# Kernel optimization log

Hardware: AMD Instinct MI355X
Metric: run time of the kernel (lower is better)

## Reference

```python
import jax, jax.numpy as jnp
import numpy as np

IN_F, OUT_F, N_PAIRS, BATCH = 1024, 1024, 4096, 32768
EPS = 1e-5

def setup_inputs() -> dict:
    key = jax.random.key(0)
    ks = jax.random.split(key, 8)
    x = jax.random.normal(ks[0], (BATCH, IN_F), dtype=jnp.float32)
    idx_i = jax.random.randint(ks[1], (N_PAIRS,), 0, IN_F)
    idx_j = jax.random.randint(ks[2], (N_PAIRS,), 0, IN_F)
    bound_lc = 1.0 / np.sqrt(N_PAIRS)
    bound_w1 = 1.0 / np.sqrt(IN_F)
    lw = jax.random.uniform(ks[3], (OUT_F, N_PAIRS), minval=-bound_lc, maxval=bound_lc, dtype=jnp.float32)
    w1 = jax.random.uniform(ks[4], (OUT_F, IN_F), minval=-bound_w1, maxval=bound_w1, dtype=jnp.float32)
    scale = jnp.ones((1, IN_F), dtype=jnp.float32)
    translation = jnp.zeros((1, IN_F), dtype=jnp.float32)
    gamma = jnp.ones((OUT_F,), dtype=jnp.float32)
    beta = jnp.zeros((OUT_F,), dtype=jnp.float32)
    return {"x": x, "idx_i": idx_i, "idx_j": idx_j, "scale": scale,
            "translation": translation, "lw": lw, "w1": w1,
            "gamma": gamma, "beta": beta}

def reference(x, idx_i, idx_j, scale, translation, lw, w1, gamma, beta):
    # levicivita transform: affine-normalize, gather pairs, multiply, GEMM
    xs = (x - translation) / scale                       # [B, in]
    pp = xs[:, idx_i] * xs[:, idx_j]                     # [B, num_pairs]
    lc = pp @ lw.T                                       # [B, out]
    base = x @ w1.T                                      # [B, out]
    c = lc + base
    # LayerNorm over last dim (eps=1e-5, biased variance, as torch)
    mu = jnp.mean(c, axis=-1, keepdims=True)
    var = jnp.mean(jnp.square(c - mu), axis=-1, keepdims=True)
    return (c - mu) * jax.lax.rsqrt(var + EPS) * gamma + beta
```

## Files before the change

### kernel.cpp

```cpp
#include <hip/hip_runtime.h>
#include <hip/hip_bf16.h>
#include <stdint.h>


#define IN_F 1024
#define OUT_F 1024
#define N_PAIRS 4096
#define BATCH_N 32768
#define KTOT (N_PAIRS + IN_F)
#define EPS_LN 1e-5f

#define BM 256
#define BN 256
#define BK 64
#define NKT (KTOT / BK)
#define RS ((size_t)KTOT * 2)

typedef __attribute__((ext_vector_type(8))) __bf16 bf16x8;
typedef __attribute__((ext_vector_type(4))) float f32x4;

__device__ __forceinline__ unsigned short f32_to_bf16_bits(float f) {
  union { float f; unsigned u; } c; c.f = f;
  unsigned r = c.u + 0x7FFFu + ((c.u >> 16) & 1u);
  return (unsigned short)(r >> 16);
}

__device__ __forceinline__ float bf16_bits_to_f32(unsigned short b) {
  union { unsigned u; float f; } c; c.u = ((unsigned)b) << 16;
  return c.f;
}

__device__ __forceinline__ void gload_lds16(const void* g, void* l) {
  __builtin_amdgcn_global_load_lds(
      (const __attribute__((address_space(1))) void*)g,
      (__attribute__((address_space(3))) void*)l, 16, 0, 0);
}

__global__ __launch_bounds__(256) void prep_w_kernel(
    const float* __restrict__ lw, const float* __restrict__ w1,
    unsigned short* __restrict__ Wcat) {
  int t = blockIdx.x * 256 + threadIdx.x;
  int e = t * 4;
  int o = e / KTOT;
  int k = e - o * KTOT;
  const float* src = (k < N_PAIRS) ? (lw + (size_t)o * N_PAIRS + k)
                                   : (w1 + (size_t)o * IN_F + (k - N_PAIRS));
  float4 v = *reinterpret_cast<const float4*>(src);
  ushort4 b;
  b.x = f32_to_bf16_bits(v.x);
  b.y = f32_to_bf16_bits(v.y);
  b.z = f32_to_bf16_bits(v.z);
  b.w = f32_to_bf16_bits(v.w);
  *reinterpret_cast<ushort4*>(Wcat + e) = b;
}

__global__ __launch_bounds__(256) void prep_x_kernel(
    const float* __restrict__ x,
    const int* __restrict__ idx_i, const int* __restrict__ idx_j,
    const float* __restrict__ scale, const float* __restrict__ translation,
    unsigned short* __restrict__ Xcat, int rowBase) {
  __shared__ float xs[IN_F];
  int r = blockIdx.x;
  int t = threadIdx.x;
  const float* xrow = x + (size_t)(rowBase + r) * IN_F;
  float4 xv = reinterpret_cast<const float4*>(xrow)[t];
  float4 sv = reinterpret_cast<const float4*>(scale)[t];
  float4 tv = reinterpret_cast<const float4*>(translation)[t];
  float4 xsv;
  xsv.x = (xv.x - tv.x) / sv.x;
  xsv.y = (xv.y - tv.y) / sv.y;
  xsv.z = (xv.z - tv.z) / sv.z;
  xsv.w = (xv.w - tv.w) / sv.w;
  reinterpret_cast<float4*>(xs)[t] = xsv;

  unsigned short* rowout = Xcat + (size_t)r * KTOT;
  ushort4 xb;
  xb.x = f32_to_bf16_bits(xv.x);
  xb.y = f32_to_bf16_bits(xv.y);
  xb.z = f32_to_bf16_bits(xv.z);
  xb.w = f32_to_bf16_bits(xv.w);
  *reinterpret_cast<ushort4*>(rowout + N_PAIRS + t * 4) = xb;

  __syncthreads();
#pragma unroll
  for (int g = 0; g < 2; ++g) {
    int p = (g * 256 + t) * 8;
    int4 ia = *reinterpret_cast<const int4*>(idx_i + p);
    int4 ib = *reinterpret_cast<const int4*>(idx_i + p + 4);
    int4 ja = *reinterpret_cast<const int4*>(idx_j + p);
    int4 jb = *reinterpret_cast<const int4*>(idx_j + p + 4);
    ushort4 oa, ob;
    oa.x = f32_to_bf16_bits(xs[ia.x] * xs[ja.x]);
    oa.y = f32_to_bf16_bits(xs[ia.y] * xs[ja.y]);
    oa.z = f32_to_bf16_bits(xs[ia.z] * xs[ja.z]);
    oa.w = f32_to_bf16_bits(xs[ia.w] * xs[ja.w]);
    ob.x = f32_to_bf16_bits(xs[ib.x] * xs[jb.x]);
    ob.y = f32_to_bf16_bits(xs[ib.y] * xs[jb.y]);
    ob.z = f32_to_bf16_bits(xs[ib.z] * xs[jb.z]);
    ob.w = f32_to_bf16_bits(xs[ib.w] * xs[jb.w]);
    *reinterpret_cast<ushort4*>(rowout + p) = oa;
    *reinterpret_cast<ushort4*>(rowout + p + 4) = ob;
  }
}


#define STAGE_HALF(h_)                                                        \
  {                                                                           \
    int h__ = (h_);                                                           \
    if (h__ < 4 * NKT) {                                                      \
      int kt__ = h__ >> 2, rg__ = h__ & 3;                                    \
      const char* mb__ = (rg__ < 2) ? Bb : Ab;                                \
      const char* src__ = mb__ + (size_t)((rg__ & 1) * 128 + srow) * RS +     \
                          (size_t)kt__ * 128 + skb;                           \
      char* dst__ = lds + ((kt__ & 1) << 16) + (rg__ << 14) + (w << 10);      \
      gload_lds16(src__, dst__);                                              \
      gload_lds16(src__ + (size_t)64 * RS, dst__ + 8192);                     \
    }                                                                         \
  }

#define MFMA_Q(mb, amv, bv)                                                   \
  __builtin_amdgcn_s_setprio(1);                                              \
  _Pragma("unroll") for (int i_ = 0; i_ < 4; ++i_)                            \
      _Pragma("unroll") for (int n_ = 0; n_ < 4; ++n_)                        \
    acc[(mb) + i_][n_] = __builtin_amdgcn_mfma_f32_16x16x32_bf16(             \
        amv[i_], bv[n_], acc[(mb) + i_][n_], 0, 0, 0);                        \
  __builtin_amdgcn_s_setprio(0);

#define KTILE_BODY(ktv, bo)                                                   \
  {                                                                           \
    const int kt_c = (ktv);                                                   \
    bf16x8 bf0[4], bf1[4], a0[4], a1[4], a2[4], a3[4];                        \
           \
    _Pragma("unroll") for (int n = 0; n < 4; ++n)                             \
        bf0[n] = *(const bf16x8*)(bRow + (bo) + n * 2048 + kb0);              \
    _Pragma("unroll") for (int i = 0; i < 4; ++i)                             \
        a0[i] = *(const bf16x8*)(aRow + (bo) + i * 2048 + kb0);               \
    STAGE_HALF(4 * (kt_c + 1) + 2);                                           \
    MFMA_Q(0, a0, bf0);                                                       \
    _Pragma("unroll") for (int n = 0; n < 4; ++n)                             \
        bf1[n] = *(const bf16x8*)(bRow + (bo) + n * 2048 + kb1);              \
    _Pragma("unroll") for (int i = 0; i < 4; ++i)                             \
        a1[i] = *(const bf16x8*)(aRow + (bo) + i * 2048 + kb1);               \
    __builtin_amdgcn_s_barrier();                                             \
                         \
    MFMA_Q(0, a1, bf1);                                                       \
    _Pragma("unroll") for (int i = 0; i < 4; ++i)                             \
        a2[i] = *(const bf16x8*)(aRow + (bo) + (4 + i) * 2048 + kb0);         \
    STAGE_HALF(4 * (kt_c + 1) + 3);                                           \
    __builtin_amdgcn_s_barrier();                                             \
                         \
    MFMA_Q(4, a2, bf0);                                                       \
    _Pragma("unroll") for (int i = 0; i < 4; ++i)                             \
        a3[i] = *(const bf16x8*)(aRow + (bo) + (4 + i) * 2048 + kb1);         \
    STAGE_HALF(4 * (kt_c + 2) + 0);                                           \
    __builtin_amdgcn_s_barrier();                                             \
                     \
    MFMA_Q(4, a3, bf1);                                                       \
    STAGE_HALF(4 * (kt_c + 2) + 1);                                           \
    if (kt_c + 2 < NKT) {                                                     \
      asm volatile("s_waitcnt vmcnt(4)" ::: "memory");                        \
    } else if (kt_c + 1 < NKT) {                                              \
      asm volatile("s_waitcnt vmcnt(0)" ::: "memory");                        \
    }                                                                         \
    __builtin_amdgcn_s_barrier();                                             \
  }

__global__ __launch_bounds__(512, 2) void gemm_kernel(
    const unsigned short* __restrict__ A,
    const unsigned short* __restrict__ Bw,
    unsigned short* __restrict__ Cb) {
  __shared__ __align__(16) char lds[131072];

  int nwg = gridDim.x;
  int bid = blockIdx.x;
  int cpx = nwg >> 3;
  int swz = (bid & 7) * cpx + (bid >> 3);
  int rt = swz >> 2;
  int ct = swz & 3;

  int tid = threadIdx.x;
  int lane = tid & 63;
  int w = tid >> 6;
  int wr = w >> 2;
  int wc = w & 3;

  const char* Ab = (const char*)A + (size_t)rt * BM * RS;
  const char* Bb = (const char*)Bw + (size_t)ct * BN * RS;

  int srow = tid >> 3;
  int skb = ((tid & 7) << 4) ^ (((tid >> 3) & 7) << 4);

  int lane15 = lane & 15;
  int cb = lane >> 4;
  int swzm = (lane15 & 7) << 4;
  int kb0 = (cb << 4) ^ swzm;
  int kb1 = (64 + (cb << 4)) ^ swzm;
  const char* aRow = lds + 32768 + (wr * 128 + lane15) * 128;
  const char* bRow = lds + (wc * 64 + lane15) * 128;

  f32x4 acc[8][4];
#pragma unroll
  for (int m = 0; m < 8; ++m)
#pragma unroll
    for (int n = 0; n < 4; ++n) acc[m][n] = {0.f, 0.f, 0.f, 0.f};

#pragma unroll
  for (int hp = 0; hp < 6; ++hp) {
    STAGE_HALF(hp);
    __builtin_amdgcn_sched_barrier(0);
  }
  asm volatile("s_waitcnt vmcnt(4)" ::: "memory");
  __builtin_amdgcn_s_barrier();

  for (int kt = 0; kt < NKT; kt += 2) {
    KTILE_BODY(kt, 0);
    KTILE_BODY(kt + 1, 65536);
  }

  int crow0 = rt * BM + wr * 128 + (cb << 2);
  int ccol0 = ct * BN + wc * 64 + lane15;
#pragma unroll
  for (int m = 0; m < 8; ++m)
#pragma unroll
    for (int n = 0; n < 4; ++n)
#pragma unroll
      for (int j = 0; j < 4; ++j)
        Cb[(size_t)(crow0 + m * 16 + j) * OUT_F + ccol0 + n * 16] =
            f32_to_bf16_bits(acc[m][n][j]);
}

__global__ __launch_bounds__(256) void ln_kernel(
    const unsigned short* __restrict__ Cb, float* __restrict__ out,
    const float* __restrict__ gamma, const float* __restrict__ beta) {
  int r = blockIdx.x;
  int t = threadIdx.x;
  ushort4 u = reinterpret_cast<const ushort4*>(Cb + (size_t)r * OUT_F)[t];
  float4 v;
  v.x = bf16_bits_to_f32(u.x);
  v.y = bf16_bits_to_f32(u.y);
  v.z = bf16_bits_to_f32(u.z);
  v.w = bf16_bits_to_f32(u.w);
  float s = v.x + v.y + v.z + v.w;
  float s2 = v.x * v.x + v.y * v.y + v.z * v.z + v.w * v.w;
#pragma unroll
  for (int off = 32; off > 0; off >>= 1) {
    s += __shfl_down(s, off, 64);
    s2 += __shfl_down(s2, off, 64);
  }
  __shared__ float ps[4], ps2[4];
  int lane = t & 63, wid = t >> 6;
  if (lane == 0) { ps[wid] = s; ps2[wid] = s2; }
  __syncthreads();
  float fs = ps[0] + ps[1] + ps[2] + ps[3];
  float fs2 = ps2[0] + ps2[1] + ps2[2] + ps2[3];
  float mu = fs * (1.0f / OUT_F);
  float var = fs2 * (1.0f / OUT_F) - mu * mu;
  float rstd = rsqrtf(var + EPS_LN);
  float4 g = reinterpret_cast<const float4*>(gamma)[t];
  float4 b = reinterpret_cast<const float4*>(beta)[t];
  float4 o;
  o.x = (v.x - mu) * rstd * g.x + b.x;
  o.y = (v.y - mu) * rstd * g.y + b.y;
  o.z = (v.z - mu) * rstd * g.z + b.z;
  o.w = (v.w - mu) * rstd * g.w + b.w;
  reinterpret_cast<float4*>(out + (size_t)r * OUT_F)[t] = o;
}

extern "C" void kernel_launch(void* const* d_in, const int* in_sizes, int n_in,
                              void* d_out, int out_size, void* d_ws, size_t ws_size,
                              hipStream_t stream) {
  const float* x           = (const float*)d_in[0];
  const int*   idx_i       = (const int*)d_in[1];
  const int*   idx_j       = (const int*)d_in[2];
  const float* scale       = (const float*)d_in[3];
  const float* translation = (const float*)d_in[4];
  const float* lw          = (const float*)d_in[5];
  const float* w1          = (const float*)d_in[6];
  const float* gamma       = (const float*)d_in[7];
  const float* beta        = (const float*)d_in[8];
  float* out = (float*)d_out;

  unsigned short* Wcat = (unsigned short*)d_ws;
  size_t wcat_bytes = (size_t)OUT_F * KTOT * 2;
  size_t avail = ws_size > wcat_bytes ? ws_size - wcat_bytes : 0;

  int chunk = BATCH_N;
  while (chunk > 512 && (size_t)chunk * (KTOT * 2 + OUT_F * 2) > avail) chunk >>= 1;

  unsigned short* Cb = (unsigned short*)((char*)d_ws + wcat_bytes);
  unsigned short* Xcat = Cb + (size_t)chunk * OUT_F;

  prep_w_kernel<<<dim3(OUT_F * KTOT / 4 / 256), dim3(256), 0, stream>>>(lw, w1, Wcat);

  for (int rb = 0; rb < BATCH_N; rb += chunk) {
    prep_x_kernel<<<dim3(chunk), dim3(256), 0, stream>>>(
        x, idx_i, idx_j, scale, translation, Xcat, rb);
    gemm_kernel<<<dim3((chunk / BM) * (OUT_F / BN)), dim3(512), 0, stream>>>(
        Xcat, Wcat, Cb);
    ln_kernel<<<dim3(chunk), dim3(256), 0, stream>>>(
        Cb, out + (size_t)rb * OUT_F, gamma, beta);
  }
}
```

Measured before the change: 421.7 us.

## Switch GEMM inner loop to 32x32x16 bf16 MFMA tiles

Replaces the 16x16x32 MFMA micro-tiles with 32x32x16 instructions, regrouping per-wave accumulators into 4x2 blocks of 16-float vectors and rewriting the LDS fragment loads and output store mapping to match. The larger MFMA shape cuts the number of LDS fragment reads per FLOP and raises per-instruction work. It also caps the batch chunk at 16384 rows, which splits the run into at least two prep/GEMM/LN passes and may change cache behaviour of the intermediate buffers.

```diff
diff --git a/kernel.cpp b/kernel.cpp
--- a/kernel.cpp
+++ b/kernel.cpp
@@ -17,7 +17,7 @@
 #define RS ((size_t)KTOT * 2)
 
 typedef __attribute__((ext_vector_type(8))) __bf16 bf16x8;
-typedef __attribute__((ext_vector_type(4))) float f32x4;
+typedef __attribute__((ext_vector_type(16))) float f32x16;
 
 __device__ __forceinline__ unsigned short f32_to_bf16_bits(float f) {
   union { float f; unsigned u; } c; c.f = f;
@@ -118,44 +118,57 @@
     }                                                                         \
   }
 
-#define MFMA_Q(mb, amv, bv)                                                   \
+#define MFMA_W(mi0, av, bv)                                                   \
   __builtin_amdgcn_s_setprio(1);                                              \
-  _Pragma("unroll") for (int i_ = 0; i_ < 4; ++i_)                            \
-      _Pragma("unroll") for (int n_ = 0; n_ < 4; ++n_)                        \
-    acc[(mb) + i_][n_] = __builtin_amdgcn_mfma_f32_16x16x32_bf16(             \
-        amv[i_], bv[n_], acc[(mb) + i_][n_], 0, 0, 0);                        \
+  _Pragma("unroll") for (int m_ = 0; m_ < 2; ++m_)                            \
+      _Pragma("unroll") for (int n_ = 0; n_ < 2; ++n_)                        \
+          _Pragma("unroll") for (int q_ = 0; q_ < 2; ++q_)                    \
+    acc[(mi0) + m_][n_] = __builtin_amdgcn_mfma_f32_32x32x16_bf16(            \
+        av[m_][q_], bv[n_][q_], acc[(mi0) + m_][n_], 0, 0, 0);                \
   __builtin_amdgcn_s_setprio(0);
 
 #define KTILE_BODY(ktv, bo)                                                   \
   {                                                                           \
     const int kt_c = (ktv);                                                   \
-    bf16x8 bf0[4], bf1[4], a0[4], a1[4], a2[4], a3[4];                        \
+    bf16x8 aW[2][2], aN[2][2], b01[2][2], b23[2][2];                          \
            \
-    _Pragma("unroll") for (int n = 0; n < 4; ++n)                             \
-        bf0[n] = *(const bf16x8*)(bRow + (bo) + n * 2048 + kb0);              \
-    _Pragma("unroll") for (int i = 0; i < 4; ++i)                             \
-        a0[i] = *(const bf16x8*)(aRow + (bo) + i * 2048 + kb0);               \
+    _Pragma("unroll") for (int m_ = 0; m_ < 2; ++m_)                          \
+        _Pragma("unroll") for (int q_ = 0; q_ < 2; ++q_)                      \
+      aW[m_][q_] = *(const bf16x8*)(aRow + (bo) + m_ * 4096 +                 \
+                                    ((q_ << 5) ^ k0b));                       \
+    _Pragma("unroll") for (int n_ = 0; n_ < 2; ++n_)                          \
+        _Pragma("unroll") for (int q_ = 0; q_ < 2; ++q_)                      \
+      b01[n_][q_] = *(const bf16x8*)(bRow + (bo) + n_ * 4096 +                \
+                                     ((q_ << 5) ^ k0b));                      \
     STAGE_HALF(4 * (kt_c + 1) + 2);                                           \
-    MFMA_Q(0, a0, bf0);                                                       \
-    _Pragma("unroll") for (int n = 0; n < 4; ++n)                             \
-        bf1[n] = *(const bf16x8*)(bRow + (bo) + n * 2048 + kb1);              \
-    _Pragma("unroll") for (int i = 0; i < 4; ++i)                             \
-        a1[i] = *(const bf16x8*)(aRow + (bo) + i * 2048 + kb1);               \
+    MFMA_W(0, aW, b01);                                                       \
+    _Pragma("unroll") for (int m_ = 0; m_ < 2; ++m_)                          \
+        _Pragma("unroll") for (int q_ = 0; q_ < 2; ++q_)                      \
+      aN[m_][q_] = *(const bf16x8*)(aRow + (bo) + m_ * 4096 +                 \
+                                    (((q_ + 2) << 5) ^ k0b));                 \
+    _Pragma("unroll") for (int n_ = 0; n_ < 2; ++n_)                          \
+        _Pragma("unroll") for (int q_ = 0; q_ < 2; ++q_)                      \
+      b23[n_][q_] = *(const bf16x8*)(bRow + (bo) + n_ * 4096 +                \
+                                     (((q_ + 2) << 5) ^ k0b));                \
     __builtin_amdgcn_s_barrier();                                             \
-                         \
-    MFMA_Q(0, a1, bf1);                                                       \
-    _Pragma("unroll") for (int i = 0; i < 4; ++i)                             \
-        a2[i] = *(const bf16x8*)(aRow + (bo) + (4 + i) * 2048 + kb0);         \
+                   \
+    MFMA_W(0, aN, b23);                                                       \
+    _Pragma("unroll") for (int m_ = 0; m_ < 2; ++m_)                          \
+        _Pragma("unroll") for (int q_ = 0; q_ < 2; ++q_)                      \
+      aW[m_][q_] = *(const bf16x8*)(aRow + (bo) + (2 + m_) * 4096 +           \
+                                    ((q_ << 5) ^ k0b));                       \
     STAGE_HALF(4 * (kt_c + 1) + 3);                                           \
     __builtin_amdgcn_s_barrier();                                             \
-                         \
-    MFMA_Q(4, a2, bf0);                                                       \
-    _Pragma("unroll") for (int i = 0; i < 4; ++i)                             \
-        a3[i] = *(const bf16x8*)(aRow + (bo) + (4 + i) * 2048 + kb1);         \
+                   \
+    MFMA_W(2, aW, b01);                                                       \
+    _Pragma("unroll") for (int m_ = 0; m_ < 2; ++m_)                          \
+        _Pragma("unroll") for (int q_ = 0; q_ < 2; ++q_)                      \
+      aN[m_][q_] = *(const bf16x8*)(aRow + (bo) + (2 + m_) * 4096 +           \
+                                    (((q_ + 2) << 5) ^ k0b));                 \
     STAGE_HALF(4 * (kt_c + 2) + 0);                                           \
     __builtin_amdgcn_s_barrier();                                             \
-                     \
-    MFMA_Q(4, a3, bf1);                                                       \
+                   \
+    MFMA_W(2, aN, b23);                                                       \
     STAGE_HALF(4 * (kt_c + 2) + 1);                                           \
     if (kt_c + 2 < NKT) {                                                     \
       asm volatile("s_waitcnt vmcnt(4)" ::: "memory");                        \
@@ -190,19 +203,18 @@
   int srow = tid >> 3;
   int skb = ((tid & 7) << 4) ^ (((tid >> 3) & 7) << 4);
 
-  int lane15 = lane & 15;
-  int cb = lane >> 4;
-  int swzm = (lane15 & 7) << 4;
-  int kb0 = (cb << 4) ^ swzm;
-  int kb1 = (64 + (cb << 4)) ^ swzm;
-  const char* aRow = lds + 32768 + (wr * 128 + lane15) * 128;
-  const char* bRow = lds + (wc * 64 + lane15) * 128;
-
-  f32x4 acc[8][4];
-#pragma unroll
-  for (int m = 0; m < 8; ++m)
-#pragma unroll
-    for (int n = 0; n < 4; ++n) acc[m][n] = {0.f, 0.f, 0.f, 0.f};
+  int lane31 = lane & 31;
+  int k0b = ((lane >> 5) << 4) ^ ((lane & 7) << 4);
+  const char* aRow = lds + 32768 + (wr * 128 + lane31) * 128;
+  const char* bRow = lds + (wc * 64 + lane31) * 128;
+
+  f32x16 acc[4][2];
+#pragma unroll
+  for (int m = 0; m < 4; ++m)
+#pragma unroll
+    for (int n = 0; n < 2; ++n)
+#pragma unroll
+      for (int q = 0; q < 16; ++q) acc[m][n][q] = 0.f;
 
 #pragma unroll
   for (int hp = 0; hp < 6; ++hp) {
@@ -217,16 +229,18 @@
     KTILE_BODY(kt + 1, 65536);
   }
 
-  int crow0 = rt * BM + wr * 128 + (cb << 2);
-  int ccol0 = ct * BN + wc * 64 + lane15;
-#pragma unroll
-  for (int m = 0; m < 8; ++m)
-#pragma unroll
-    for (int n = 0; n < 4; ++n)
-#pragma unroll
-      for (int j = 0; j < 4; ++j)
-        Cb[(size_t)(crow0 + m * 16 + j) * OUT_F + ccol0 + n * 16] =
-            f32_to_bf16_bits(acc[m][n][j]);
+  int rbase = rt * BM + wr * 128 + 4 * (lane >> 5);
+  int cbase = ct * BN + wc * 64 + lane31;
+#pragma unroll
+  for (int mi = 0; mi < 4; ++mi)
+#pragma unroll
+    for (int ni = 0; ni < 2; ++ni)
+#pragma unroll
+      for (int rg = 0; rg < 16; ++rg) {
+        int grow = rbase + mi * 32 + (rg & 3) + 8 * (rg >> 2);
+        Cb[(size_t)grow * OUT_F + cbase + ni * 32] =
+            f32_to_bf16_bits(acc[mi][ni][rg]);
+      }
 }
 
 __global__ __launch_bounds__(256) void ln_kernel(
@@ -286,6 +300,7 @@
 
   int chunk = BATCH_N;
   while (chunk > 512 && (size_t)chunk * (KTOT * 2 + OUT_F * 2) > avail) chunk >>= 1;
+  if (chunk > 16384) chunk = 16384;
 
   unsigned short* Cb = (unsigned short*)((char*)d_ws + wcat_bytes);
   unsigned short* Xcat = Cb + (size_t)chunk * OUT_F;
```

After: 441.8 us. 1.05x slower.

## Rotate MFMA quadrants across k-tiles to overlap LDS reads with compute

Applied to the files above, without the earlier changes.

Restructures the GEMM main loop into a software-pipelined rotation. The last MFMA quadrant of each k-tile is deferred into the start of the next tile, so it overlaps with that tile's LDS fragment reads. Fragment registers are shared across iterations, and the global-to-LDS staging calls and barriers are reordered. This aims to hide LDS latency behind MFMA work, at the cost of longer register live ranges and a riskier barrier/stage ordering around the double-buffered LDS.

```diff
diff --git a/kernel.cpp b/kernel.cpp
--- a/kernel.cpp
+++ b/kernel.cpp
@@ -126,37 +126,36 @@
         amv[i_], bv[n_], acc[(mb) + i_][n_], 0, 0, 0);                        \
   __builtin_amdgcn_s_setprio(0);
 
-#define KTILE_BODY(ktv, bo)                                                   \
+#define ROT_KTILE(ktv, bo, W1M)                                               \
   {                                                                           \
     const int kt_c = (ktv);                                                   \
-    bf16x8 bf0[4], bf1[4], a0[4], a1[4], a2[4], a3[4];                        \
-           \
+               \
     _Pragma("unroll") for (int n = 0; n < 4; ++n)                             \
-        bf0[n] = *(const bf16x8*)(bRow + (bo) + n * 2048 + kb0);              \
+        B0r[n] = *(const bf16x8*)(bRow + (bo) + n * 2048 + kb0);              \
     _Pragma("unroll") for (int i = 0; i < 4; ++i)                             \
-        a0[i] = *(const bf16x8*)(aRow + (bo) + i * 2048 + kb0);               \
+        A0r[i] = *(const bf16x8*)(aRow + (bo) + i * 2048 + kb0);              \
+    if (W1M) { MFMA_Q(4, A1r, B1r); }                                         \
+    __builtin_amdgcn_s_barrier();                                             \
+                   \
+    _Pragma("unroll") for (int n = 0; n < 4; ++n)                             \
+        B1r[n] = *(const bf16x8*)(bRow + (bo) + n * 2048 + kb1);              \
+    _Pragma("unroll") for (int i = 0; i < 4; ++i)                             \
+        A1r[i] = *(const bf16x8*)(aRow + (bo) + i * 2048 + kb1);              \
     STAGE_HALF(4 * (kt_c + 1) + 2);                                           \
-    MFMA_Q(0, a0, bf0);                                                       \
-    _Pragma("unroll") for (int n = 0; n < 4; ++n)                             \
-        bf1[n] = *(const bf16x8*)(bRow + (bo) + n * 2048 + kb1);              \
+    STAGE_HALF(4 * (kt_c + 1) + 3);                                           \
+    MFMA_Q(0, A0r, B0r);                                                      \
+    __builtin_amdgcn_s_barrier();                                             \
+                 \
     _Pragma("unroll") for (int i = 0; i < 4; ++i)                             \
-        a1[i] = *(const bf16x8*)(aRow + (bo) + i * 2048 + kb1);               \
+        A0r[i] = *(const bf16x8*)(aRow + (bo) + (4 + i) * 2048 + kb0);        \
+    STAGE_HALF(4 * (kt_c + 2) + 0);                                           \
+    MFMA_Q(0, A1r, B1r);                                                      \
     __builtin_amdgcn_s_barrier();                                             \
-                         \
-    MFMA_Q(0, a1, bf1);                                                       \
+        \
     _Pragma("unroll") for (int i = 0; i < 4; ++i)                             \
-        a2[i] = *(const bf16x8*)(aRow + (bo) + (4 + i) * 2048 + kb0);         \
-    STAGE_HALF(4 * (kt_c + 1) + 3);                                           \
-    __builtin_amdgcn_s_barrier();                                             \
-                         \
-    MFMA_Q(4, a2, bf0);                                                       \
-    _Pragma("unroll") for (int i = 0; i < 4; ++i)                             \
-        a3[i] = *(const bf16x8*)(aRow + (bo) + (4 + i) * 2048 + kb1);         \
-    STAGE_HALF(4 * (kt_c + 2) + 0);                                           \
-    __builtin_amdgcn_s_barrier();                                             \
-                     \
-    MFMA_Q(4, a3, bf1);                                                       \
+        A1r[i] = *(const bf16x8*)(aRow + (bo) + (4 + i) * 2048 + kb1);        \
     STAGE_HALF(4 * (kt_c + 2) + 1);                                           \
+    MFMA_Q(4, A0r, B0r);                                                      \
     if (kt_c + 2 < NKT) {                                                     \
       asm volatile("s_waitcnt vmcnt(4)" ::: "memory");                        \
     } else if (kt_c + 1 < NKT) {                                              \
@@ -204,6 +203,8 @@
 #pragma unroll
     for (int n = 0; n < 4; ++n) acc[m][n] = {0.f, 0.f, 0.f, 0.f};
 
+  bf16x8 A0r[4], A1r[4], B0r[4], B1r[4];
+
 #pragma unroll
   for (int hp = 0; hp < 6; ++hp) {
     STAGE_HALF(hp);
@@ -212,10 +213,13 @@
   asm volatile("s_waitcnt vmcnt(4)" ::: "memory");
   __builtin_amdgcn_s_barrier();
 
-  for (int kt = 0; kt < NKT; kt += 2) {
-    KTILE_BODY(kt, 0);
-    KTILE_BODY(kt + 1, 65536);
-  }
+  ROT_KTILE(0, 0, 0);
+  ROT_KTILE(1, 65536, 1);
+  for (int kt = 2; kt < NKT; kt += 2) {
+    ROT_KTILE(kt, 0, 1);
+    ROT_KTILE(kt + 1, 65536, 1);
+  }
+  MFMA_Q(4, A1r, B1r);
 
   int crow0 = rt * BM + wr * 128 + (cb << 2);
   int ccol0 = ct * BN + wc * 64 + lane15;
```

Measured after the change: 681.4 us. 1.62x slower.
